# Performance work log

Hardware: AMD Instinct MI355X
Metric: run time of the kernel (lower is better)

## Reference

```python
import jax, jax.numpy as jnp
import numpy as np


def setup_inputs() -> dict:
    key = jax.random.key(0)
    ks = jax.random.split(key, 16)
    B, C, H, W = 2, 64, 512, 512
    Nl, Nr = 100000, 20000

    def lin(k, fan_in, fan_out):
        kw, kb = jax.random.split(k)
        bound = 1.0 / np.sqrt(fan_in)
        w = jax.random.uniform(kw, (fan_in, fan_out), jnp.float32, -bound, bound)
        b = jax.random.uniform(kb, (fan_out,), jnp.float32, -bound, bound)
        return w, b

    w_lin, b_lin = lin(ks[0], 128, 64)
    w1, b1 = lin(ks[1], 128, 64)
    w2, b2 = lin(ks[2], 64, 32)
    w3, b3 = lin(ks[3], 32, 16)
    w4, b4 = lin(ks[4], 16, 1)

    return {
        "pc0_map": jax.random.normal(ks[5], (B, C, H, W), jnp.float32),
        "pc1_map": jax.random.normal(ks[6], (B, C, H, W), jnp.float32),
        "flow_map": jax.random.normal(ks[7], (B, C, H, W), jnp.float32),
        "lidar_coords": jax.random.randint(ks[8], (B, Nl, 3), 0, 512).astype(jnp.int64),
        "radar_coords": jax.random.randint(ks[9], (B, Nr, 3), 0, 512).astype(jnp.int64),
        "w_lin": w_lin, "b_lin": b_lin,
        "w1": w1, "b1": b1, "w2": w2, "b2": b2,
        "w3": w3, "b3": b3, "w4": w4, "b4": b4,
    }


def reference(pc0_map, pc1_map, flow_map, lidar_coords, radar_coords,
              w_lin, b_lin, w1, b1, w2, b2, w3, b3, w4, b4):
    gelu = lambda x: jax.nn.gelu(x, approximate=False)  # torch nn.GELU default (erf)

    def seg_single(p0, p1, fl, lc, rc):
        # lc: [Nl,3], rc: [Nr,3]; cat(lidar, radar) for all three maps
        coords = jnp.concatenate([lc, rc], axis=0)        # [N,3]
        r, c = coords[:, 1], coords[:, 2]
        f0 = p0[:, r, c].T                                # [N,64]
        f1 = p1[:, r, c].T                                # [N,64]
        ff = fl[:, r, c].T                                # [N,64]
        pc = jnp.concatenate([f0, f1], axis=1) @ w_lin + b_lin   # [N,64]
        h = jnp.concatenate([pc, ff], axis=1)             # [N,128]
        h = gelu(h @ w1 + b1)
        h = gelu(h @ w2 + b2)
        h = gelu(h @ w3 + b3)
        s = jax.nn.sigmoid(h @ w4 + b4)                   # [N,1]
        return s[:, 0]

    # [B, Nl+Nr] stacked (original returns a per-batch list; fixed N lets us stack)
    return jax.vmap(seg_single)(pc0_map, pc1_map, flow_map, lidar_coords, radar_coords)
```

## Files before the change

kernel.cpp:

```cpp
#include <hip/hip_runtime.h>
#include <math.h>

#define NPTS 120000
#define NLID 100000
#define NRAD 20000
#define NTOT (2 * NPTS)
#define MAPW 512
#define MAPHW (512 * 512)
#define NTILES 8192

typedef short sh8 __attribute__((ext_vector_type(8)));
typedef float f32x4 __attribute__((ext_vector_type(4)));
typedef unsigned short u16;
typedef unsigned int u32;

#define CSTR 70
#define H1S 72
#define H2S 40
#define H3S 24
#define HWAVE (16 * (H1S + H2S + H3S))

__device__ __forceinline__ float gelu_f(float x) {
    return 0.5f * x * (1.0f + erff(x * 0.7071067811865476f));
}
__device__ __forceinline__ u16 f2bf(float f) {
    unsigned int u = __float_as_uint(f);
    return (u16)((u + 0x7FFFu + ((u >> 16) & 1u)) >> 16);
}
__device__ __forceinline__ float bf2f(u16 h) {
    return __uint_as_float((unsigned int)h << 16);
}

__global__ void wprep_kernel(const float* __restrict__ w_lin, const float* __restrict__ b_lin,
                             const float* __restrict__ w1, const float* __restrict__ b1,
                             const float* __restrict__ w2, const float* __restrict__ w3,
                             u16* __restrict__ wfrag1, u16* __restrict__ wfrag2,
                             u16* __restrict__ wfrag3, float* __restrict__ b_eff) {
    int e = blockIdx.x * blockDim.x + threadIdx.x;
    if (e < 12288) {
        int fi = e >> 9, r = e & 511, lane = r >> 3, j = r & 7;
        int kk = fi >> 2, nt = fi & 3;
        int k = kk * 32 + (lane >> 4) * 8 + j;
        int n = nt * 16 + (lane & 15);
        float val;
        if (k < 128) {
            float s = 0.f;
            for (int jj = 0; jj < 64; jj++) s += w_lin[k * 64 + jj] * w1[jj * 64 + n];
            val = s;
        } else {
            val = w1[(k - 64) * 64 + n];
        }
        wfrag1[e] = f2bf(val);
    } else if (e < 12288 + 2048) {
        int e2 = e - 12288;
        int fi = e2 >> 9, lane = (e2 >> 3) & 63, j = e2 & 7;
        int kk = fi >> 1, nt = fi & 1;
        int k = kk * 32 + (lane >> 4) * 8 + j;
        int n = nt * 16 + (lane & 15);
        wfrag2[e2] = f2bf(w2[k * 32 + n]);
    } else if (e < 12288 + 2048 + 512) {
        int e3 = e - 12288 - 2048;
        int lane = e3 >> 3, j = e3 & 7;
        int k = (lane >> 4) * 8 + j;
        int n = lane & 15;
        wfrag3[e3] = f2bf(w3[k * 16 + n]);
    } else if (e < 12288 + 2048 + 512 + 64) {
        int n = e - 12288 - 2048 - 512;
        float s = b1[n];
        for (int jj = 0; jj < 64; jj++) s += b_lin[jj] * w1[jj * 64 + n];
        b_eff[n] = s;
    }
}

__global__ __launch_bounds__(256, 6) void fbseg_dense_kernel(
    const float* __restrict__ p0, const float* __restrict__ p1,
    const float* __restrict__ fl,
    const u16* __restrict__ wfrag1, const u16* __restrict__ wfrag2,
    const u16* __restrict__ wfrag3, const float* __restrict__ b_eff,
    const float* __restrict__ b2, const float* __restrict__ b3,
    const float* __restrict__ w4, const float* __restrict__ b4,
    float* __restrict__ score)
{
    __shared__ __align__(16) u16 feat[192 * CSTR];

    const int tid  = threadIdx.x;
    const int wv   = tid >> 6;
    const int lane = tid & 63;
    const int lr   = lane & 15;
    const int lq   = lane >> 4;
    const int m0w  = wv * 16;
    const int col  = m0w + lr;

    const int nb = blockIdx.x;
    const int b  = nb >> 12;
    const int r  = (nb & 4095) >> 3;
    const int c0 = (nb & 7) << 6;

    {
        const int q  = lq;
        const int p4 = lr * 4;
        const unsigned laneoff = (unsigned)(q * MAPHW + p4);
        f32x4 v[12];
        #pragma unroll
        for (int s = 0; s < 12; s++) {
            const int C4s = __builtin_amdgcn_readfirstlane(wv * 48 + s * 4);
            const float* mp = (C4s < 64) ? p0 : ((C4s < 128) ? p1 : fl);
            const float* bs = mp + (size_t)b * ((size_t)64 * MAPHW)
                            + (size_t)(C4s & 63) * MAPHW
                            + (size_t)r * MAPW + (size_t)c0;
            v[s] = *(const f32x4*)(bs + laneoff);
        }
        #pragma unroll
        for (int s = 0; s < 12; s++) {
            const int C = wv * 48 + s * 4 + q;
            u32 lo, hi;
            asm("v_cvt_pk_bf16_f32 %0, %1, %2" : "=v"(lo) : "v"(v[s][0]), "v"(v[s][1]));
            asm("v_cvt_pk_bf16_f32 %0, %1, %2" : "=v"(hi) : "v"(v[s][2]), "v"(v[s][3]));
            u32* dst = (u32*)(feat + C * CSTR + p4);
            dst[0] = lo;
            dst[1] = hi;
        }
    }
    __syncthreads();

    f32x4 acc1[4] = {};
    #pragma unroll
    for (int kk = 0; kk < 6; kk++) {
        sh8 a;
        u16* ap = (u16*)&a;
        #pragma unroll
        for (int j = 0; j < 8; j++)
            ap[j] = feat[(kk * 32 + lq * 8 + j) * CSTR + col];
        #pragma unroll
        for (int nt = 0; nt < 4; nt++) {
            sh8 bfr = *(const sh8*)(wfrag1 + ((kk * 4 + nt) * 64 + lane) * 8);
            acc1[nt] = __builtin_amdgcn_mfma_f32_16x16x32_bf16(a, bfr, acc1[nt], 0, 0, 0);
        }
    }
    __syncthreads();

    u16* Hbase = feat + wv * HWAVE;
    u16* H1w = Hbase;
    u16* H2w = Hbase + 16 * H1S;
    u16* H3w = Hbase + 16 * H1S + 16 * H2S;

    #pragma unroll
    for (int nt = 0; nt < 4; nt++) {
        const int n = nt * 16 + lr;
        const float bias = b_eff[n];
        #pragma unroll
        for (int rg = 0; rg < 4; rg++) {
            const int row = lq * 4 + rg;
            H1w[row * H1S + n] = f2bf(gelu_f(acc1[nt][rg] + bias));
        }
    }

    f32x4 acc2[2] = {};
    #pragma unroll
    for (int kk = 0; kk < 2; kk++) {
        sh8 a = *(const sh8*)&H1w[lr * H1S + kk * 32 + lq * 8];
        #pragma unroll
        for (int nt = 0; nt < 2; nt++) {
            sh8 bfr = *(const sh8*)(wfrag2 + ((kk * 2 + nt) * 64 + lane) * 8);
            acc2[nt] = __builtin_amdgcn_mfma_f32_16x16x32_bf16(a, bfr, acc2[nt], 0, 0, 0);
        }
    }
    #pragma unroll
    for (int nt = 0; nt < 2; nt++) {
        const int n = nt * 16 + lr;
        const float bias = b2[n];
        #pragma unroll
        for (int rg = 0; rg < 4; rg++) {
            const int row = lq * 4 + rg;
            H2w[row * H2S + n] = f2bf(gelu_f(acc2[nt][rg] + bias));
        }
    }

    f32x4 acc3 = {};
    {
        sh8 a = *(const sh8*)&H2w[lr * H2S + lq * 8];
        sh8 bfr = *(const sh8*)(wfrag3 + lane * 8);
        acc3 = __builtin_amdgcn_mfma_f32_16x16x32_bf16(a, bfr, acc3, 0, 0, 0);
    }
    {
        const float bias = b3[lr];
        #pragma unroll
        for (int rg = 0; rg < 4; rg++) {
            const int row = lq * 4 + rg;
            H3w[row * H3S + lr] = f2bf(gelu_f(acc3[rg] + bias));
        }
    }

    if (lane < 16) {
        float s = b4[0];
        #pragma unroll
        for (int k = 0; k < 16; k++) s = fmaf(bf2f(H3w[lane * H3S + k]), w4[k], s);
        score[(size_t)b * MAPHW + (size_t)r * MAPW + (size_t)(c0 + m0w + lane)] =
            1.0f / (1.0f + expf(-s));
    }
}

__global__ void lookup_kernel(const int* __restrict__ lidar, const int* __restrict__ radar,
                              const float* __restrict__ score, float* __restrict__ out) {
    int p = blockIdx.x * blockDim.x + threadIdx.x;
    if (p >= NTOT) return;
    int b = p / NPTS;
    int i = p - b * NPTS;
    int r, c;
    if (i < NLID) {
        const int* cd = lidar + (size_t)(b * NLID + i) * 3;
        r = cd[1]; c = cd[2];
    } else {
        const int* cd = radar + (size_t)(b * NRAD + (i - NLID)) * 3;
        r = cd[1]; c = cd[2];
    }
    out[p] = score[(size_t)b * MAPHW + (size_t)r * MAPW + (size_t)c];
}

extern "C" void kernel_launch(void* const* d_in, const int* in_sizes, int n_in,
                              void* d_out, int out_size, void* d_ws, size_t ws_size,
                              hipStream_t stream) {
    const float* p0    = (const float*)d_in[0];
    const float* p1    = (const float*)d_in[1];
    const float* fl    = (const float*)d_in[2];
    const int*   lidar = (const int*)d_in[3];
    const int*   radar = (const int*)d_in[4];
    const float* w_lin = (const float*)d_in[5];
    const float* b_lin = (const float*)d_in[6];
    const float* w1    = (const float*)d_in[7];
    const float* b1    = (const float*)d_in[8];
    const float* w2    = (const float*)d_in[9];
    const float* b2    = (const float*)d_in[10];
    const float* w3    = (const float*)d_in[11];
    const float* b3    = (const float*)d_in[12];
    const float* w4    = (const float*)d_in[13];
    const float* b4    = (const float*)d_in[14];
    float* out = (float*)d_out;

    char* ws = (char*)d_ws;
    float* score = (float*)ws;
    char* wbase  = ws + (size_t)2 * MAPHW * sizeof(float);
    u16*  wfrag1 = (u16*)wbase;
    u16*  wfrag2 = (u16*)(wbase + 12288 * 2);
    u16*  wfrag3 = (u16*)(wbase + (12288 + 2048) * 2);
    float* b_eff = (float*)(wbase + (12288 + 2048 + 512) * 2);

    hipLaunchKernelGGL(wprep_kernel, dim3((14912 + 255) / 256), dim3(256), 0, stream,
                       w_lin, b_lin, w1, b1, w2, w3, wfrag1, wfrag2, wfrag3, b_eff);
    hipLaunchKernelGGL(fbseg_dense_kernel, dim3(NTILES), dim3(256), 0, stream,
                       p0, p1, fl, wfrag1, wfrag2, wfrag3, b_eff, b2, b3, w4, b4, score);
    hipLaunchKernelGGL(lookup_kernel, dim3((NTOT + 255) / 256), dim3(256), 0, stream,
                       lidar, radar, score, out);
}
```

Before: 398.8 us.

## Process four tiles per block with register prefetch of next tile

Each block now handles four consecutive 64-pixel tiles. The global loads for the next tile are issued into registers while the current tile's MLP runs, overlapping memory latency with compute. This costs more VGPRs, so launch bounds drop from 6 to 4 blocks per CU, and the grid shrinks by 4x, which reduces parallelism and occupancy.

Result: slower. 433.7 us (+8.7%).

```diff
diff --git a/kernel.cpp b/kernel.cpp
--- a/kernel.cpp
+++ b/kernel.cpp
@@ -8,6 +8,8 @@
 #define MAPW 512
 #define MAPHW (512 * 512)
 #define NTILES 8192
+#define TPB 4
+#define NBLK (NTILES / TPB)
 
 typedef short sh8 __attribute__((ext_vector_type(8)));
 typedef float f32x4 __attribute__((ext_vector_type(4)));
@@ -72,7 +74,40 @@
     }
 }
 
-__global__ __launch_bounds__(256, 6) void fbseg_dense_kernel(
+__device__ __forceinline__ void load_tile(f32x4* v, int nb, int wv, int lq, int lr,
+                                          const float* __restrict__ p0,
+                                          const float* __restrict__ p1,
+                                          const float* __restrict__ fl) {
+    const int b  = nb >> 12;
+    const int r  = (nb & 4095) >> 3;
+    const int c0 = (nb & 7) << 6;
+    const int laneoff = lq * MAPHW + lr * 4;
+    #pragma unroll
+    for (int s = 0; s < 12; s++) {
+        const int C4s = __builtin_amdgcn_readfirstlane(wv * 48 + s * 4);
+        const float* mp = (C4s < 64) ? p0 : ((C4s < 128) ? p1 : fl);
+        const float* bs = mp + (size_t)b * ((size_t)64 * MAPHW)
+                        + (size_t)(C4s & 63) * MAPHW
+                        + (size_t)r * MAPW + (size_t)c0;
+        v[s] = *(const f32x4*)(bs + laneoff);
+    }
+}
+
+__device__ __forceinline__ void store_tile(const f32x4* v, u16* feat, int wv, int lq, int lr) {
+    const int p4 = lr * 4;
+    #pragma unroll
+    for (int s = 0; s < 12; s++) {
+        const int C = wv * 48 + s * 4 + lq;
+        u32 lo, hi;
+        asm("v_cvt_pk_bf16_f32 %0, %1, %2" : "=v"(lo) : "v"(v[s][0]), "v"(v[s][1]));
+        asm("v_cvt_pk_bf16_f32 %0, %1, %2" : "=v"(hi) : "v"(v[s][2]), "v"(v[s][3]));
+        u32* dst = (u32*)(feat + C * CSTR + p4);
+        dst[0] = lo;
+        dst[1] = hi;
+    }
+}
+
+__global__ __launch_bounds__(256, 4) void fbseg_dense_kernel(
     const float* __restrict__ p0, const float* __restrict__ p1,
     const float* __restrict__ fl,
     const u16* __restrict__ wfrag1, const u16* __restrict__ wfrag2,
@@ -91,112 +126,106 @@
     const int m0w  = wv * 16;
     const int col  = m0w + lr;
 
-    const int nb = blockIdx.x;
-    const int b  = nb >> 12;
-    const int r  = (nb & 4095) >> 3;
-    const int c0 = (nb & 7) << 6;
-
-    {
-        const int q  = lq;
-        const int p4 = lr * 4;
-        const unsigned laneoff = (unsigned)(q * MAPHW + p4);
-        f32x4 v[12];
-        #pragma unroll
-        for (int s = 0; s < 12; s++) {
-            const int C4s = __builtin_amdgcn_readfirstlane(wv * 48 + s * 4);
-            const float* mp = (C4s < 64) ? p0 : ((C4s < 128) ? p1 : fl);
-            const float* bs = mp + (size_t)b * ((size_t)64 * MAPHW)
-                            + (size_t)(C4s & 63) * MAPHW
-                            + (size_t)r * MAPW + (size_t)c0;
-            v[s] = *(const f32x4*)(bs + laneoff);
-        }
-        #pragma unroll
-        for (int s = 0; s < 12; s++) {
-            const int C = wv * 48 + s * 4 + q;
-            u32 lo, hi;
-            asm("v_cvt_pk_bf16_f32 %0, %1, %2" : "=v"(lo) : "v"(v[s][0]), "v"(v[s][1]));
-            asm("v_cvt_pk_bf16_f32 %0, %1, %2" : "=v"(hi) : "v"(v[s][2]), "v"(v[s][3]));
-            u32* dst = (u32*)(feat + C * CSTR + p4);
-            dst[0] = lo;
-            dst[1] = hi;
-        }
-    }
-    __syncthreads();
-
-    f32x4 acc1[4] = {};
-    #pragma unroll
-    for (int kk = 0; kk < 6; kk++) {
-        sh8 a;
-        u16* ap = (u16*)&a;
-        #pragma unroll
-        for (int j = 0; j < 8; j++)
-            ap[j] = feat[(kk * 32 + lq * 8 + j) * CSTR + col];
-        #pragma unroll
-        for (int nt = 0; nt < 4; nt++) {
-            sh8 bfr = *(const sh8*)(wfrag1 + ((kk * 4 + nt) * 64 + lane) * 8);
-            acc1[nt] = __builtin_amdgcn_mfma_f32_16x16x32_bf16(a, bfr, acc1[nt], 0, 0, 0);
-        }
-    }
-    __syncthreads();
+    const int nb0 = blockIdx.x * TPB;
 
     u16* Hbase = feat + wv * HWAVE;
     u16* H1w = Hbase;
     u16* H2w = Hbase + 16 * H1S;
     u16* H3w = Hbase + 16 * H1S + 16 * H2S;
 
+    f32x4 v[12];
+    load_tile(v, nb0, wv, lq, lr, p0, p1, fl);
+
     #pragma unroll
-    for (int nt = 0; nt < 4; nt++) {
-        const int n = nt * 16 + lr;
-        const float bias = b_eff[n];
-        #pragma unroll
-        for (int rg = 0; rg < 4; rg++) {
-            const int row = lq * 4 + rg;
-            H1w[row * H1S + n] = f2bf(gelu_f(acc1[nt][rg] + bias));
-        }
-    }
-
-    f32x4 acc2[2] = {};
-    #pragma unroll
-    for (int kk = 0; kk < 2; kk++) {
-        sh8 a = *(const sh8*)&H1w[lr * H1S + kk * 32 + lq * 8];
+    for (int t = 0; t < TPB; t++) {
+        const int nb = nb0 + t;
+
+        store_tile(v, feat, wv, lq, lr);
+        __syncthreads();
+
+        f32x4 vn[12];
+        if (t < TPB - 1) load_tile(vn, nb + 1, wv, lq, lr, p0, p1, fl);
+
+        f32x4 acc1[4] = {};
+        #pragma unroll
+        for (int kk = 0; kk < 6; kk++) {
+            sh8 a;
+            u16* ap = (u16*)&a;
+            #pragma unroll
+            for (int j = 0; j < 8; j++)
+                ap[j] = feat[(kk * 32 + lq * 8 + j) * CSTR + col];
+            #pragma unroll
+            for (int nt = 0; nt < 4; nt++) {
+                sh8 bfr = *(const sh8*)(wfrag1 + ((kk * 4 + nt) * 64 + lane) * 8);
+                acc1[nt] = __builtin_amdgcn_mfma_f32_16x16x32_bf16(a, bfr, acc1[nt], 0, 0, 0);
+            }
+        }
+        __syncthreads();
+
+        #pragma unroll
+        for (int nt = 0; nt < 4; nt++) {
+            const int n = nt * 16 + lr;
+            const float bias = b_eff[n];
+            #pragma unroll
+            for (int rg = 0; rg < 4; rg++) {
+                const int row = lq * 4 + rg;
+                H1w[row * H1S + n] = f2bf(gelu_f(acc1[nt][rg] + bias));
+            }
+        }
+
+        f32x4 acc2[2] = {};
+        #pragma unroll
+        for (int kk = 0; kk < 2; kk++) {
+            sh8 a = *(const sh8*)&H1w[lr * H1S + kk * 32 + lq * 8];
+            #pragma unroll
+            for (int nt = 0; nt < 2; nt++) {
+                sh8 bfr = *(const sh8*)(wfrag2 + ((kk * 2 + nt) * 64 + lane) * 8);
+                acc2[nt] = __builtin_amdgcn_mfma_f32_16x16x32_bf16(a, bfr, acc2[nt], 0, 0, 0);
+            }
+        }
         #pragma unroll
         for (int nt = 0; nt < 2; nt++) {
-            sh8 bfr = *(const sh8*)(wfrag2 + ((kk * 2 + nt) * 64 + lane) * 8);
-            acc2[nt] = __builtin_amdgcn_mfma_f32_16x16x32_bf16(a, bfr, acc2[nt], 0, 0, 0);
-        }
-    }
-    #pragma unroll
-    for (int nt = 0; nt < 2; nt++) {
-        const int n = nt * 16 + lr;
-        const float bias = b2[n];
-        #pragma unroll
-        for (int rg = 0; rg < 4; rg++) {
-            const int row = lq * 4 + rg;
-            H2w[row * H2S + n] = f2bf(gelu_f(acc2[nt][rg] + bias));
-        }
-    }
-
-    f32x4 acc3 = {};
-    {
-        sh8 a = *(const sh8*)&H2w[lr * H2S + lq * 8];
-        sh8 bfr = *(const sh8*)(wfrag3 + lane * 8);
-        acc3 = __builtin_amdgcn_mfma_f32_16x16x32_bf16(a, bfr, acc3, 0, 0, 0);
-    }
-    {
-        const float bias = b3[lr];
-        #pragma unroll
-        for (int rg = 0; rg < 4; rg++) {
-            const int row = lq * 4 + rg;
-            H3w[row * H3S + lr] = f2bf(gelu_f(acc3[rg] + bias));
-        }
-    }
-
-    if (lane < 16) {
-        float s = b4[0];
-        #pragma unroll
-        for (int k = 0; k < 16; k++) s = fmaf(bf2f(H3w[lane * H3S + k]), w4[k], s);
-        score[(size_t)b * MAPHW + (size_t)r * MAPW + (size_t)(c0 + m0w + lane)] =
-            1.0f / (1.0f + expf(-s));
+            const int n = nt * 16 + lr;
+            const float bias = b2[n];
+            #pragma unroll
+            for (int rg = 0; rg < 4; rg++) {
+                const int row = lq * 4 + rg;
+                H2w[row * H2S + n] = f2bf(gelu_f(acc2[nt][rg] + bias));
+            }
+        }
+
+        f32x4 acc3 = {};
+        {
+            sh8 a = *(const sh8*)&H2w[lr * H2S + lq * 8];
+            sh8 bfr = *(const sh8*)(wfrag3 + lane * 8);
+            acc3 = __builtin_amdgcn_mfma_f32_16x16x32_bf16(a, bfr, acc3, 0, 0, 0);
+        }
+        {
+            const float bias = b3[lr];
+            #pragma unroll
+            for (int rg = 0; rg < 4; rg++) {
+                const int row = lq * 4 + rg;
+                H3w[row * H3S + lr] = f2bf(gelu_f(acc3[rg] + bias));
+            }
+        }
+
+        if (lane < 16) {
+            float s = b4[0];
+            #pragma unroll
+            for (int k = 0; k < 16; k++) s = fmaf(bf2f(H3w[lane * H3S + k]), w4[k], s);
+            const int b  = nb >> 12;
+            const int r  = (nb & 4095) >> 3;
+            const int c0 = (nb & 7) << 6;
+            score[(size_t)b * MAPHW + (size_t)r * MAPW + (size_t)(c0 + m0w + lane)] =
+                1.0f / (1.0f + expf(-s));
+        }
+
+        __syncthreads();
+
+        if (t < TPB - 1) {
+            #pragma unroll
+            for (int s = 0; s < 12; s++) v[s] = vn[s];
+        }
     }
 }
 
@@ -247,7 +276,7 @@
 
     hipLaunchKernelGGL(wprep_kernel, dim3((14912 + 255) / 256), dim3(256), 0, stream,
                        w_lin, b_lin, w1, b1, w2, w3, wfrag1, wfrag2, wfrag3, b_eff);
-    hipLaunchKernelGGL(fbseg_dense_kernel, dim3(NTILES), dim3(256), 0, stream,
+    hipLaunchKernelGGL(fbseg_dense_kernel, dim3(NBLK), dim3(256), 0, stream,
                        p0, p1, fl, wfrag1, wfrag2, wfrag3, b_eff, b2, b3, w4, b4, score);
     hipLaunchKernelGGL(lookup_kernel, dim3((NTOT + 255) / 256), dim3(256), 0, stream,
                        lidar, radar, score, out);
```
